# Performance work log

Hardware: AMD Instinct MI355X
Metric: run time of the kernel (lower is better)

Reference implementation:

```python
import jax, jax.numpy as jnp
import numpy as np

V = 500_000
NF = 1_000_000
K_DEG = 7


def _build_mesh_ops(rng):
    faces = rng.integers(0, V, size=(NF, 3), dtype=np.int64)
    f0, f1, f2 = faces[:, 0], faces[:, 1], faces[:, 2]
    rows = np.concatenate([f0, f1, f1, f2, f2, f0])
    cols = np.concatenate([f1, f0, f2, f1, f0, f2])
    keep = rows != cols
    rows, cols = rows[keep], cols[keep]
    code = np.unique(rows * V + cols)  # dedupe symmetric edge list
    rows_u = (code // V).astype(np.int32)
    cols_u = (code % V).astype(np.int32)
    deg = np.bincount(rows_u, minlength=V).astype(np.float32)
    deg = np.maximum(deg, 1.0)
    off_vals = (1.0 / deg[rows_u]).astype(np.float32)
    diag = np.arange(V, dtype=np.int32)
    lap_rows = np.concatenate([rows_u, diag])
    lap_cols = np.concatenate([cols_u, diag])
    lap_vals = np.concatenate([off_vals, -np.ones(V, dtype=np.float32)])
    # sparse hexagon operator K: ~7 nnz per row
    k_rows = np.repeat(np.arange(V, dtype=np.int32), K_DEG)
    k_cols = rng.integers(0, V, size=V * K_DEG).astype(np.int32)
    k_vals = (rng.standard_normal(V * K_DEG) * 0.1).astype(np.float32)
    return faces.astype(np.int32), lap_rows, lap_cols, lap_vals, k_rows, k_cols, k_vals


def setup_inputs() -> dict:
    key = jax.random.key(0)
    rng = np.random.default_rng(0)
    faces, lap_rows, lap_cols, lap_vals, k_rows, k_cols, k_vals = _build_mesh_ops(rng)
    vertices = jax.random.normal(key, (V, 3), dtype=jnp.float32)
    return {
        "vertices": vertices,
        "center": jnp.zeros((1, 3), dtype=jnp.float32),
        "lap_rows": jnp.asarray(lap_rows),
        "lap_cols": jnp.asarray(lap_cols),
        "lap_vals": jnp.asarray(lap_vals),
        "k_rows": jnp.asarray(k_rows),
        "k_cols": jnp.asarray(k_cols),
        "k_vals": jnp.asarray(k_vals),
        "faces": jnp.asarray(faces),
        "total_num": 4,
    }


def _spmv3(rows, cols, vals, verts, n):
    # sparse [n,n] COO matmul with [n,3] verts
    gathered = vals[:, None] * verts[cols]  # [nnz,3]
    return jax.ops.segment_sum(gathered, rows, num_segments=n)


def reference(vertices, center, lap_rows, lap_cols, lap_vals,
              k_rows, k_cols, k_vals, faces, total_num):
    n = vertices.shape[0]
    verts = vertices + center  # [V,3], broadcast of [1,3] center
    # uniform laplacian smoothing loss: mean_i ||(L v)_i||_2
    lap_out = _spmv3(lap_rows, lap_cols, lap_vals, verts, n)
    laplacian_loss = jnp.mean(jnp.linalg.norm(lap_out, axis=1))
    # hexagon regularity loss: mean_i ||(K v)_i||^2
    k_out = _spmv3(k_rows, k_cols, k_vals, verts, n)
    hexagon_loss = jnp.mean(jnp.sum(k_out * k_out, axis=1))
    vertices_rep = jnp.tile(verts[None], (total_num, 1, 1))
    faces_rep = jnp.tile(faces[None], (total_num, 1, 1))
    zero = jnp.zeros((), dtype=verts.dtype)
    return (vertices_rep, faces_rep, laplacian_loss, hexagon_loss, zero, zero)
```

## Files before the change

kernel.cpp:

```cpp
#include <hip/hip_runtime.h>
#include <hip/hip_fp16.h>
#include <math.h>

#define BLK  256
#define KDEG 7
#define CHB  24
#define CH2  8

typedef float    fvec4 __attribute__((ext_vector_type(4)));
typedef int      ivec4 __attribute__((ext_vector_type(4)));
typedef int      ivec2 __attribute__((ext_vector_type(2)));
typedef unsigned uvec4 __attribute__((ext_vector_type(4)));

#define H16(x) ((unsigned)__half_as_ushort(__float2half(x)))

__global__ void prep_kernel(const fvec4* __restrict__ vin,
                            const float* __restrict__ center,
                            const ivec4* __restrict__ faces,
                            float* __restrict__ out,
                            ushort4* __restrict__ v16,
                            int* __restrict__ bounds,
                            long scalar_base,
                            int V4, int n4v, int n4f, long frep_q,
                            int T, int nbv) {
    if ((int)blockIdx.x < nbv) {
        int r4 = blockIdx.x * BLK + threadIdx.x;
        if (r4 == 0) {
            out[scalar_base + 0] = 0.f;
            out[scalar_base + 1] = 0.f;
            out[scalar_base + 2] = 0.f;
            out[scalar_base + 3] = 0.f;
        }
        if (r4 >= V4) return;
        float c0 = center[0], c1 = center[1], c2 = center[2];
        long qb = 3L * r4;
        fvec4 a = __builtin_nontemporal_load(&vin[qb]);
        fvec4 b = __builtin_nontemporal_load(&vin[qb + 1]);
        fvec4 c = __builtin_nontemporal_load(&vin[qb + 2]);
        a.x += c0; a.y += c1; a.z += c2; a.w += c0;
        b.x += c1; b.y += c2; b.z += c0; b.w += c1;
        c.x += c2; c.y += c0; c.z += c1; c.w += c2;
#pragma unroll 4
        for (int t = 0; t < T; ++t) {
            fvec4* o = (fvec4*)out + (long)t * n4v + qb;
            __builtin_nontemporal_store(a, o);
            __builtin_nontemporal_store(b, o + 1);
            __builtin_nontemporal_store(c, o + 2);
        }
        uvec4 p0, p1;
        p0.x = H16(a.x) | (H16(a.y) << 16);
        p0.y = H16(a.z);
        p0.z = H16(a.w) | (H16(b.x) << 16);
        p0.w = H16(b.y);
        p1.x = H16(b.z) | (H16(b.w) << 16);
        p1.y = H16(c.x);
        p1.z = H16(c.y) | (H16(c.z) << 16);
        p1.w = H16(c.w);
        uvec4* vp = (uvec4*)(v16 + 4L * r4);
        vp[0] = p0; vp[1] = p1;
        uvec4 z = {0u, 0u, 0u, 0u};
        uvec4* bp = (uvec4*)(bounds + 8L * r4);
        bp[0] = z; bp[1] = z;
    } else {
        int i = ((int)blockIdx.x - nbv) * BLK + threadIdx.x;
        if (i >= n4f) return;
        ivec4 f = __builtin_nontemporal_load(&faces[i]);
        fvec4 g;
        g.x = (float)f.x; g.y = (float)f.y; g.z = (float)f.z; g.w = (float)f.w;
        fvec4* o = (fvec4*)out + frep_q;
#pragma unroll 4
        for (int t = 0; t < T; ++t)
            __builtin_nontemporal_store(g, &o[(long)t * n4f + i]);
    }
}

__global__ void row_bounds_kernel(const int* __restrict__ rows,
                                  int* __restrict__ bnd,
                                  int nnz_off) {
    int j = blockIdx.x * blockDim.x + threadIdx.x;
    if (j >= nnz_off) return;
    int r = rows[j];
    if (j == 0) {
        bnd[2 * r] = 0;
    } else {
        int rp = rows[j - 1];
        if (rp != r) {
            bnd[2 * r] = j;
            bnd[2 * rp + 1] = j;
        }
    }
    if (j == nnz_off - 1) bnd[2 * r + 1] = nnz_off;
}

__device__ __forceinline__ float2 block_reduce_sum2(float2 v) {
    for (int o = 32; o > 0; o >>= 1) {
        v.x += __shfl_down(v.x, o, 64);
        v.y += __shfl_down(v.y, o, 64);
    }
    __shared__ float2 s[BLK / 64];
    int lane = threadIdx.x & 63;
    int wid  = threadIdx.x >> 6;
    if (lane == 0) s[wid] = v;
    __syncthreads();
    if (wid == 0) {
        v = (lane < BLK / 64) ? s[lane] : make_float2(0.f, 0.f);
        for (int o = (BLK / 64) / 2; o > 0; o >>= 1) {
            v.x += __shfl_down(v.x, o, 64);
            v.y += __shfl_down(v.y, o, 64);
        }
    }
    return v;
}

__launch_bounds__(BLK, 4)
__global__ void fused_loss_kernel(const ivec2* __restrict__ bounds,
                                  const int* __restrict__ cols,
                                  const int* __restrict__ kcols,
                                  const float* __restrict__ kvals,
                                  const ushort4* __restrict__ v16,
                                  int V, float invV,
                                  float* __restrict__ acc ) {
    const int r   = blockIdx.x * BLK + threadIdx.x;
    const bool act = (r < V);
    const int rr  = act ? r : 0;

    ivec2 be = __builtin_nontemporal_load(&bounds[rr]);
    int lo = be.x, hi = be.y;
    if (!act) { lo = 0; hi = 0; }
    const int cnt = hi - lo;

    long kb = (long)rr * KDEG;
    int   kc[KDEG]; float kv[KDEG];
#pragma unroll
    for (int t = 0; t < KDEG; ++t) kc[t] = __builtin_nontemporal_load(&kcols[kb + t]);
#pragma unroll
    for (int t = 0; t < KDEG; ++t) kv[t] = __builtin_nontemporal_load(&kvals[kb + t]);

    ushort4 ur = v16[rr];

    ushort4 ku[KDEG];
#pragma unroll
    for (int t = 0; t < KDEG; ++t) ku[t] = v16[kc[t]];

    int m0 = cnt < CHB ? cnt : CHB;
    int cc[CHB];
#pragma unroll
    for (int t = 0; t < CHB; ++t) cc[t] = __builtin_nontemporal_load(&cols[lo + t]);

    ushort4 cu[CHB];
#pragma unroll
    for (int t = 0; t < CHB; ++t) {
        int ct = (t < m0) ? cc[t] : 0;
        cu[t] = v16[ct];
    }

    float qx = 0.f, qy = 0.f, qz = 0.f;
#pragma unroll
    for (int t = 0; t < KDEG; ++t) {
        qx += kv[t] * __half2float(__ushort_as_half(ku[t].x));
        qy += kv[t] * __half2float(__ushort_as_half(ku[t].y));
        qz += kv[t] * __half2float(__ushort_as_half(ku[t].z));
    }

    float sx = 0.f, sy = 0.f, sz = 0.f;
#pragma unroll
    for (int t = 0; t < CHB; ++t) {
        float hx = __half2float(__ushort_as_half(cu[t].x));
        float hy = __half2float(__ushort_as_half(cu[t].y));
        float hz = __half2float(__ushort_as_half(cu[t].z));
        sx += (t < m0) ? hx : 0.f;
        sy += (t < m0) ? hy : 0.f;
        sz += (t < m0) ? hz : 0.f;
    }

    for (int j = lo + CHB; j < hi; j += CH2) {
        int m = hi - j; if (m > CH2) m = CH2;
        int c2[CH2];
#pragma unroll
        for (int t = 0; t < CH2; ++t) c2[t] = __builtin_nontemporal_load(&cols[j + t]);
        ushort4 u2[CH2];
#pragma unroll
        for (int t = 0; t < CH2; ++t) {
            int ct = (t < m) ? c2[t] : 0;
            u2[t] = v16[ct];
        }
#pragma unroll
        for (int t = 0; t < CH2; ++t) {
            float hx = __half2float(__ushort_as_half(u2[t].x));
            float hy = __half2float(__ushort_as_half(u2[t].y));
            float hz = __half2float(__ushort_as_half(u2[t].z));
            sx += (t < m) ? hx : 0.f;
            sy += (t < m) ? hy : 0.f;
            sz += (t < m) ? hz : 0.f;
        }
    }

    float2 contrib = make_float2(0.f, 0.f);
    if (act) {
        float vx = __half2float(__ushort_as_half(ur.x));
        float vy = __half2float(__ushort_as_half(ur.y));
        float vz = __half2float(__ushort_as_half(ur.z));
        float inv = (cnt > 0) ? 1.f / (float)cnt : 0.f;
        float lx = sx * inv - vx;
        float ly = sy * inv - vy;
        float lz = sz * inv - vz;
        contrib.x = sqrtf(lx * lx + ly * ly + lz * lz) * invV;
        contrib.y = (qx * qx + qy * qy + qz * qz) * invV;
    }
    float2 s = block_reduce_sum2(contrib);
    if (threadIdx.x == 0) {
        atomicAdd(&acc[0], s.x);
        atomicAdd(&acc[1], s.y);
    }
}

__global__ void finalize_kernel(float* __restrict__ scal, float invV) {
    scal[0] *= invV;
    scal[1] *= invV;
}

__global__ void vrep_scalar(const float* __restrict__ vertices,
                            const float* __restrict__ center,
                            float* __restrict__ out, int V3, int T) {
    int i = blockIdx.x * blockDim.x + threadIdx.x;
    if (i >= V3) return;
    float v = vertices[i] + center[i % 3];
    for (int t = 0; t < T; ++t) out[(long)t * V3 + i] = v;
}

__global__ void frep_scalar(const int* __restrict__ faces,
                            float* __restrict__ out, int NF3, int T) {
    int i = blockIdx.x * blockDim.x + threadIdx.x;
    if (i >= NF3) return;
    float f = (float)faces[i];
    for (int t = 0; t < T; ++t) out[(long)t * NF3 + i] = f;
}

__global__ void zero_scal_kernel(float* __restrict__ scal) {
    scal[0] = 0.f; scal[1] = 0.f; scal[2] = 0.f; scal[3] = 0.f;
}

__global__ void lap_loss_fb(const int* __restrict__ rows,
                            const int* __restrict__ cols,
                            const float* __restrict__ vals,
                            const float* __restrict__ verts,
                            int nnz_off, int V, float* __restrict__ acc) {
    int r = blockIdx.x * blockDim.x + threadIdx.x;
    float contrib = 0.f;
    if (r < V) {
        int lo = 0, hi = nnz_off;
        while (lo < hi) { int mid = (lo + hi) >> 1; if (rows[mid] < r) lo = mid + 1; else hi = mid; }
        float sx = 0.f, sy = 0.f, sz = 0.f;
        for (int j = lo; j < nnz_off; ++j) {
            if (rows[j] != r) break;
            float v = vals[j]; long c = (long)cols[j] * 3;
            sx += v * verts[c]; sy += v * verts[c + 1]; sz += v * verts[c + 2];
        }
        float dv = vals[nnz_off + r]; long c = (long)r * 3;
        sx += dv * verts[c]; sy += dv * verts[c + 1]; sz += dv * verts[c + 2];
        contrib = sqrtf(sx * sx + sy * sy + sz * sz);
    }
    float2 s = block_reduce_sum2(make_float2(contrib, 0.f));
    if (threadIdx.x == 0) atomicAdd(acc, s.x);
}

__global__ void k_loss_fb(const int* __restrict__ kcols,
                          const float* __restrict__ kvals,
                          const float* __restrict__ verts,
                          int V, int K, float* __restrict__ acc) {
    int r = blockIdx.x * blockDim.x + threadIdx.x;
    float contrib = 0.f;
    if (r < V) {
        long base = (long)r * K;
        float sx = 0.f, sy = 0.f, sz = 0.f;
        for (int j = 0; j < K; ++j) {
            float v = kvals[base + j]; long c = (long)kcols[base + j] * 3;
            sx += v * verts[c]; sy += v * verts[c + 1]; sz += v * verts[c + 2];
        }
        contrib = sx * sx + sy * sy + sz * sz;
    }
    float2 s = block_reduce_sum2(make_float2(contrib, 0.f));
    if (threadIdx.x == 0) atomicAdd(acc, s.x);
}

extern "C" void kernel_launch(void* const* d_in, const int* in_sizes, int n_in,
                              void* d_out, int out_size, void* d_ws, size_t ws_size,
                              hipStream_t stream) {
    const float* vertices = (const float*)d_in[0];
    const float* center   = (const float*)d_in[1];
    const int*   lap_rows = (const int*)d_in[2];
    const int*   lap_cols = (const int*)d_in[3];
    const float* lap_vals = (const float*)d_in[4];
    const int*   k_cols   = (const int*)d_in[6];
    const float* k_vals   = (const float*)d_in[7];
    const int*   faces    = (const int*)d_in[8];

    float* out = (float*)d_out;

    const int V3      = in_sizes[0];
    const int V       = V3 / 3;
    const int nnz     = in_sizes[2];
    const int nnz_off = nnz - V;
    const int K       = in_sizes[7] / V;
    const int NF3     = in_sizes[8];
    const long scalar_base = (long)out_size - 4;
    const int T = (int)(((long)out_size - 4) / ((long)V3 + (long)NF3));

    const size_t need = (size_t)V * (8 + 8);
    int*     bounds = (int*)d_ws;
    ushort4* v16    = (ushort4*)(bounds + 2L * V);

    const bool fast = (ws_size >= need) && (K == KDEG) &&
                      ((V3 & 3) == 0) && ((NF3 & 3) == 0) && ((V & 3) == 0) &&
                      (V >= 2 * CHB);

    if (fast) {
        const int V4  = V >> 2;
        const int n4v = V3 >> 2;
        const int n4f = NF3 >> 2;
        const int nbv = (V4 + BLK - 1) / BLK;
        const int nbf = (n4f + BLK - 1) / BLK;
        const long frep_q = (long)T * n4v;

        prep_kernel<<<nbv + nbf, BLK, 0, stream>>>(
            (const fvec4*)vertices, center, (const ivec4*)faces, out,
            v16, bounds, scalar_base, V4, n4v, n4f, frep_q, T, nbv);

        row_bounds_kernel<<<(nnz_off + BLK - 1) / BLK, BLK, 0, stream>>>(
            lap_rows, bounds, nnz_off);

        fused_loss_kernel<<<(V + BLK - 1) / BLK, BLK, 0, stream>>>(
            (const ivec2*)bounds, lap_cols, k_cols, k_vals, v16,
            V, 1.0f / (float)V, out + scalar_base);
    } else {
        zero_scal_kernel<<<1, 1, 0, stream>>>(out + scalar_base);
        vrep_scalar<<<(V3 + BLK - 1) / BLK, BLK, 0, stream>>>(
            vertices, center, out, V3, T);
        frep_scalar<<<(NF3 + BLK - 1) / BLK, BLK, 0, stream>>>(
            faces, out + (long)T * V3, NF3, T);
        lap_loss_fb<<<(V + BLK - 1) / BLK, BLK, 0, stream>>>(
            lap_rows, lap_cols, lap_vals, out, nnz_off, V, out + scalar_base);
        k_loss_fb<<<(V + BLK - 1) / BLK, BLK, 0, stream>>>(
            k_cols, k_vals, out, V, K, out + scalar_base + 1);
        finalize_kernel<<<1, 1, 0, stream>>>(out + scalar_base, 1.0f / (float)V);
    }
}
```

Measured before the change: 255.9 us.

## Split each row's gather work across two lanes with shuffle reduction

Each Laplacian and K row is now handled by two adjacent threads instead of one. They interleave the neighbor and K-column indices, each gathers half the fp16 vertices, and the partial sums are combined with __shfl_xor. The launch doubles the thread count. The goal is to cut per-thread register arrays and load latency chains, raising occupancy and memory-level parallelism. In exchange it duplicates the bounds and row-vertex loads, leaves half the threads idle in the final step, and adds dummy K loads for the odd lane.

```diff
diff --git a/kernel.cpp b/kernel.cpp
--- a/kernel.cpp
+++ b/kernel.cpp
@@ -5,7 +5,9 @@
 #define BLK  256
 #define KDEG 7
 #define CHB  24
+#define CHT  12
 #define CH2  8
+#define CHT2 4
 
 typedef float    fvec4 __attribute__((ext_vector_type(4)));
 typedef int      ivec4 __attribute__((ext_vector_type(4)));
@@ -120,7 +122,9 @@
                                   const ushort4* __restrict__ v16,
                                   int V, float invV,
                                   float* __restrict__ acc ) {
-    const int r   = blockIdx.x * BLK + threadIdx.x;
+    const int gid = blockIdx.x * BLK + threadIdx.x;
+    const int r   = gid >> 1;
+    const int h   = gid & 1;
     const bool act = (r < V);
     const int rr  = act ? r : 0;
 
@@ -130,44 +134,51 @@
     const int cnt = hi - lo;
 
     long kb = (long)rr * KDEG;
-    int   kc[KDEG]; float kv[KDEG];
-#pragma unroll
-    for (int t = 0; t < KDEG; ++t) kc[t] = __builtin_nontemporal_load(&kcols[kb + t]);
-#pragma unroll
-    for (int t = 0; t < KDEG; ++t) kv[t] = __builtin_nontemporal_load(&kvals[kb + t]);
+    int   kc[CHT2]; float kv[CHT2];
+#pragma unroll
+    for (int u = 0; u < CHT2; ++u) {
+        int t = h + 2 * u; int tt = (t < KDEG) ? t : 0;
+        kc[u] = __builtin_nontemporal_load(&kcols[kb + tt]);
+        kv[u] = __builtin_nontemporal_load(&kvals[kb + tt]);
+    }
 
     ushort4 ur = v16[rr];
 
-    ushort4 ku[KDEG];
-#pragma unroll
-    for (int t = 0; t < KDEG; ++t) ku[t] = v16[kc[t]];
+    ushort4 ku[CHT2];
+#pragma unroll
+    for (int u = 0; u < CHT2; ++u) ku[u] = v16[kc[u]];
 
     int m0 = cnt < CHB ? cnt : CHB;
-    int cc[CHB];
-#pragma unroll
-    for (int t = 0; t < CHB; ++t) cc[t] = __builtin_nontemporal_load(&cols[lo + t]);
-
-    ushort4 cu[CHB];
-#pragma unroll
-    for (int t = 0; t < CHB; ++t) {
-        int ct = (t < m0) ? cc[t] : 0;
-        cu[t] = v16[ct];
+    int cc[CHT];
+#pragma unroll
+    for (int u = 0; u < CHT; ++u)
+        cc[u] = __builtin_nontemporal_load(&cols[lo + h + 2 * u]);
+
+    ushort4 cu[CHT];
+#pragma unroll
+    for (int u = 0; u < CHT; ++u) {
+        int t = h + 2 * u;
+        int ct = (t < m0) ? cc[u] : 0;
+        cu[u] = v16[ct];
     }
 
     float qx = 0.f, qy = 0.f, qz = 0.f;
 #pragma unroll
-    for (int t = 0; t < KDEG; ++t) {
-        qx += kv[t] * __half2float(__ushort_as_half(ku[t].x));
-        qy += kv[t] * __half2float(__ushort_as_half(ku[t].y));
-        qz += kv[t] * __half2float(__ushort_as_half(ku[t].z));
+    for (int u = 0; u < CHT2; ++u) {
+        int t = h + 2 * u;
+        float w = (t < KDEG) ? kv[u] : 0.f;
+        qx += w * __half2float(__ushort_as_half(ku[u].x));
+        qy += w * __half2float(__ushort_as_half(ku[u].y));
+        qz += w * __half2float(__ushort_as_half(ku[u].z));
     }
 
     float sx = 0.f, sy = 0.f, sz = 0.f;
 #pragma unroll
-    for (int t = 0; t < CHB; ++t) {
-        float hx = __half2float(__ushort_as_half(cu[t].x));
-        float hy = __half2float(__ushort_as_half(cu[t].y));
-        float hz = __half2float(__ushort_as_half(cu[t].z));
+    for (int u = 0; u < CHT; ++u) {
+        int t = h + 2 * u;
+        float hx = __half2float(__ushort_as_half(cu[u].x));
+        float hy = __half2float(__ushort_as_half(cu[u].y));
+        float hz = __half2float(__ushort_as_half(cu[u].z));
         sx += (t < m0) ? hx : 0.f;
         sy += (t < m0) ? hy : 0.f;
         sz += (t < m0) ? hz : 0.f;
@@ -175,28 +186,38 @@
 
     for (int j = lo + CHB; j < hi; j += CH2) {
         int m = hi - j; if (m > CH2) m = CH2;
-        int c2[CH2];
-#pragma unroll
-        for (int t = 0; t < CH2; ++t) c2[t] = __builtin_nontemporal_load(&cols[j + t]);
-        ushort4 u2[CH2];
-#pragma unroll
-        for (int t = 0; t < CH2; ++t) {
-            int ct = (t < m) ? c2[t] : 0;
-            u2[t] = v16[ct];
-        }
-#pragma unroll
-        for (int t = 0; t < CH2; ++t) {
-            float hx = __half2float(__ushort_as_half(u2[t].x));
-            float hy = __half2float(__ushort_as_half(u2[t].y));
-            float hz = __half2float(__ushort_as_half(u2[t].z));
+        int c2[CHT2];
+#pragma unroll
+        for (int u = 0; u < CHT2; ++u)
+            c2[u] = __builtin_nontemporal_load(&cols[j + h + 2 * u]);
+        ushort4 u2[CHT2];
+#pragma unroll
+        for (int u = 0; u < CHT2; ++u) {
+            int t = h + 2 * u;
+            int ct = (t < m) ? c2[u] : 0;
+            u2[u] = v16[ct];
+        }
+#pragma unroll
+        for (int u = 0; u < CHT2; ++u) {
+            int t = h + 2 * u;
+            float hx = __half2float(__ushort_as_half(u2[u].x));
+            float hy = __half2float(__ushort_as_half(u2[u].y));
+            float hz = __half2float(__ushort_as_half(u2[u].z));
             sx += (t < m) ? hx : 0.f;
             sy += (t < m) ? hy : 0.f;
             sz += (t < m) ? hz : 0.f;
         }
     }
 
+    sx += __shfl_xor(sx, 1, 64);
+    sy += __shfl_xor(sy, 1, 64);
+    sz += __shfl_xor(sz, 1, 64);
+    qx += __shfl_xor(qx, 1, 64);
+    qy += __shfl_xor(qy, 1, 64);
+    qz += __shfl_xor(qz, 1, 64);
+
     float2 contrib = make_float2(0.f, 0.f);
-    if (act) {
+    if (act && h == 0) {
         float vx = __half2float(__ushort_as_half(ur.x));
         float vy = __half2float(__ushort_as_half(ur.y));
         float vz = __half2float(__ushort_as_half(ur.z));
@@ -329,7 +350,8 @@
         row_bounds_kernel<<<(nnz_off + BLK - 1) / BLK, BLK, 0, stream>>>(
             lap_rows, bounds, nnz_off);
 
-        fused_loss_kernel<<<(V + BLK - 1) / BLK, BLK, 0, stream>>>(
+        const long nthr = 2L * V;
+        fused_loss_kernel<<<(int)((nthr + BLK - 1) / BLK), BLK, 0, stream>>>(
             (const ivec2*)bounds, lap_cols, k_cols, k_vals, v16,
             V, 1.0f / (float)V, out + scalar_base);
     } else {
```

After: 298.3 us. +16.6%, slower.

## Stage per-block CSR column segment and K operator rows through LDS

Applied to the files above, without the earlier changes.

Each block finds the min and max CSR bounds of its rows, then loads that contiguous column segment, plus the block's K columns and values, into shared memory with coalesced strided loads. Per-thread reads then come from LDS instead of uncoalesced per-row global reads. This costs about 32 KB of LDS per block and two block barriers, which may lower occupancy under launch_bounds(BLK,4). Blocks whose segment exceeds the cap fall back to global loads.

```diff
diff --git a/kernel.cpp b/kernel.cpp
--- a/kernel.cpp
+++ b/kernel.cpp
@@ -6,6 +6,8 @@
 #define KDEG 7
 #define CHB  24
 #define CH2  8
+#define SEG_CAP 4544
+#define KSEG (BLK * KDEG)
 
 typedef float    fvec4 __attribute__((ext_vector_type(4)));
 typedef int      ivec4 __attribute__((ext_vector_type(4)));
@@ -120,7 +122,14 @@
                                   const ushort4* __restrict__ v16,
                                   int V, float invV,
                                   float* __restrict__ acc ) {
-    const int r   = blockIdx.x * BLK + threadIdx.x;
+    __shared__ int   s_cols[SEG_CAP];
+    __shared__ int   s_kc[KSEG];
+    __shared__ float s_kv[KSEG];
+    __shared__ int   s_mm[(BLK / 64) * 2];
+
+    const int R0  = blockIdx.x * BLK;
+    const int tid = threadIdx.x;
+    const int r   = R0 + tid;
     const bool act = (r < V);
     const int rr  = act ? r : 0;
 
@@ -129,12 +138,42 @@
     if (!act) { lo = 0; hi = 0; }
     const int cnt = hi - lo;
 
-    long kb = (long)rr * KDEG;
+    int lmin = (cnt > 0) ? lo : 0x7fffffff;
+    int lmax = (cnt > 0) ? hi : 0;
+    for (int o = 32; o > 0; o >>= 1) {
+        lmin = min(lmin, __shfl_xor(lmin, o, 64));
+        lmax = max(lmax, __shfl_xor(lmax, o, 64));
+    }
+    int lane = tid & 63, wid = tid >> 6;
+    if (lane == 0) { s_mm[2 * wid] = lmin; s_mm[2 * wid + 1] = lmax; }
+    __syncthreads();
+    lmin = min(min(s_mm[0], s_mm[2]), min(s_mm[4], s_mm[6]));
+    lmax = max(max(s_mm[1], s_mm[3]), max(s_mm[5], s_mm[7]));
+    const int lo_blk = lmin;
+    const int seg    = (lmax > lmin) ? (lmax - lmin) : 0;
+    const bool staged = (seg <= SEG_CAP);
+
+    if (staged) {
+        if (seg == 0) { if (tid == 0) s_cols[0] = 0; }
+        else {
+            for (int i = tid; i < seg; i += BLK)
+                s_cols[i] = __builtin_nontemporal_load(&cols[lo_blk + i]);
+        }
+    }
+    int nrows = V - R0; if (nrows > BLK) nrows = BLK;
+    const int kn = nrows * KDEG;
+    const long kbase = (long)R0 * KDEG;
+    for (int i = tid; i < kn; i += BLK) {
+        s_kc[i] = __builtin_nontemporal_load(&kcols[kbase + i]);
+        s_kv[i] = __builtin_nontemporal_load(&kvals[kbase + i]);
+    }
+    __syncthreads();
+
+    const int lr = act ? tid : 0;
+    const int kb2 = lr * KDEG;
     int   kc[KDEG]; float kv[KDEG];
 #pragma unroll
-    for (int t = 0; t < KDEG; ++t) kc[t] = __builtin_nontemporal_load(&kcols[kb + t]);
-#pragma unroll
-    for (int t = 0; t < KDEG; ++t) kv[t] = __builtin_nontemporal_load(&kvals[kb + t]);
+    for (int t = 0; t < KDEG; ++t) { kc[t] = s_kc[kb2 + t]; kv[t] = s_kv[kb2 + t]; }
 
     ushort4 ur = v16[rr];
 
@@ -142,11 +181,20 @@
 #pragma unroll
     for (int t = 0; t < KDEG; ++t) ku[t] = v16[kc[t]];
 
-    int m0 = cnt < CHB ? cnt : CHB;
+    const int m0 = cnt < CHB ? cnt : CHB;
+    const int base = lo - lo_blk;
     int cc[CHB];
-#pragma unroll
-    for (int t = 0; t < CHB; ++t) cc[t] = __builtin_nontemporal_load(&cols[lo + t]);
-
+    if (staged) {
+#pragma unroll
+        for (int t = 0; t < CHB; ++t) {
+            int idx = (t < m0) ? (base + t) : 0;
+            cc[t] = s_cols[idx];
+        }
+    } else {
+#pragma unroll
+        for (int t = 0; t < CHB; ++t)
+            cc[t] = __builtin_nontemporal_load(&cols[lo + t]);
+    }
     ushort4 cu[CHB];
 #pragma unroll
     for (int t = 0; t < CHB; ++t) {
@@ -176,8 +224,17 @@
     for (int j = lo + CHB; j < hi; j += CH2) {
         int m = hi - j; if (m > CH2) m = CH2;
         int c2[CH2];
-#pragma unroll
-        for (int t = 0; t < CH2; ++t) c2[t] = __builtin_nontemporal_load(&cols[j + t]);
+        if (staged) {
+#pragma unroll
+            for (int t = 0; t < CH2; ++t) {
+                int idx = (t < m) ? (j - lo_blk + t) : 0;
+                c2[t] = s_cols[idx];
+            }
+        } else {
+#pragma unroll
+            for (int t = 0; t < CH2; ++t)
+                c2[t] = __builtin_nontemporal_load(&cols[j + t]);
+        }
         ushort4 u2[CH2];
 #pragma unroll
         for (int t = 0; t < CH2; ++t) {
```

New measurement: 265.9 us. +3.9%, slower.
